# Optimization experiments

Measured on AMD Instinct MI355X. Metric: run time of the kernel, lower is better.

Reference implementation:

```python
import jax, jax.numpy as jnp
import numpy as np
from jax.ops import segment_sum, segment_max

N_NODES = 50000
N_GRAPHS = 64
EPS = 1e-16


def gat_layer(x, src, dst, W, a_src, a_dst, b, n_nodes):
    # PyG GATConv, heads=1: shared linear, additive attention, per-dst softmax
    h = x @ W                                  # [N, H]
    al_s = h @ a_src                           # [N]
    al_d = h @ a_dst                           # [N]
    e = jax.nn.leaky_relu(al_s[src] + al_d[dst], 0.2)   # [E]
    # numerically stable segment softmax over edges grouped by dst
    m = segment_max(e, dst, num_segments=n_nodes)
    m = jnp.where(jnp.isfinite(m), m, 0.0)
    ex = jnp.exp(e - m[dst])
    denom = segment_sum(ex, dst, num_segments=n_nodes)
    alpha = ex / (denom[dst] + EPS)            # [E]
    out = segment_sum(alpha[:, None] * h[src], dst, num_segments=n_nodes)
    return out + b


def setup_inputs() -> dict:
    key = jax.random.key(0)
    ks = jax.random.split(key, 16)
    H = 128
    x = jax.random.normal(ks[0], (N_NODES, 4), dtype=jnp.float32)
    edge_index = jax.random.randint(ks[1], (2, 800000), 0, N_NODES, dtype=jnp.int64)
    batch = jnp.sort(jax.random.randint(ks[2], (N_NODES,), 0, N_GRAPHS, dtype=jnp.int64))

    def glorot(k, shape):
        lim = np.sqrt(6.0 / (shape[0] + shape[-1]))
        return jax.random.uniform(k, shape, jnp.float32, -lim, lim)

    params = {
        'W1': glorot(ks[3], (4, H)), 'as1': glorot(ks[4], (H,)), 'ad1': glorot(ks[5], (H,)), 'b1': jnp.zeros((H,), jnp.float32),
        'W2': glorot(ks[6], (H, H)), 'as2': glorot(ks[7], (H,)), 'ad2': glorot(ks[8], (H,)), 'b2': jnp.zeros((H,), jnp.float32),
        'W3': glorot(ks[9], (H, H)), 'as3': glorot(ks[10], (H,)), 'ad3': glorot(ks[11], (H,)), 'b3': jnp.zeros((H,), jnp.float32),
        'Wlin': glorot(ks[12], (H, 2)), 'blin': jnp.zeros((2,), jnp.float32),
    }
    return {'x': x, 'edge_index': edge_index, 'batch': batch, **params}


def reference(x, edge_index, batch, W1, as1, ad1, b1, W2, as2, ad2, b2, W3, as3, ad3, b3, Wlin, blin):
    n = x.shape[0]
    # GATConv default add_self_loops=True
    loop = jnp.arange(n, dtype=edge_index.dtype)
    src = jnp.concatenate([edge_index[0], loop])
    dst = jnp.concatenate([edge_index[1], loop])

    h = jax.nn.relu(gat_layer(x, src, dst, W1, as1, ad1, b1, n))
    h = jax.nn.relu(gat_layer(h, src, dst, W2, as2, ad2, b2, n))
    h = gat_layer(h, src, dst, W3, as3, ad3, b3, n)

    # global_mean_pool
    sums = segment_sum(h, batch, num_segments=N_GRAPHS)          # [G, H]
    cnt = segment_sum(jnp.ones((n,), h.dtype), batch, num_segments=N_GRAPHS)
    pooled = sums / jnp.maximum(cnt, 1.0)[:, None]
    # dropout p=0.5 is identity in eval mode
    return pooled @ Wlin + blin                                   # [G, 2]
```

## Files before the change

kernel.cpp:

```cpp
#include <hip/hip_runtime.h>
#include <math.h>


#define BW 512
#define PART_CHUNK 4096

typedef __attribute__((ext_vector_type(8))) short short8v;
typedef __attribute__((ext_vector_type(4))) float f32x4;

__device__ __forceinline__ float bflo(unsigned u) { return __uint_as_float(u << 16); }
__device__ __forceinline__ float bfhi(unsigned u) { return __uint_as_float(u & 0xffff0000u); }
__device__ __forceinline__ unsigned pk2bf(float a, float b) {
  unsigned ua = __float_as_uint(a); ua += 0x7fffu + ((ua >> 16) & 1u);
  unsigned ub = __float_as_uint(b); ub += 0x7fffu + ((ub >> 16) & 1u);
  return (ua >> 16) | (ub & 0xffff0000u);
}

__global__ __launch_bounds__(256) void kb_hist(const int* __restrict__ ei,
                                               int* __restrict__ bcnt,
                                               int E, int ET, int NB) {
  __shared__ int h[128];
  int tid = threadIdx.x;
  if (tid < 128) h[tid] = 0;
  __syncthreads();
  int stride = gridDim.x * 256;
  for (int i = blockIdx.x * 256 + tid; i < ET; i += stride) {
    int dst = (i < E) ? ei[E + i] : (i - E);
    atomicAdd(&h[dst >> 9], 1);
  }
  __syncthreads();
  if (tid < NB && h[tid] > 0) atomicAdd(&bcnt[tid], h[tid]);
}

__global__ __launch_bounds__(128) void kb_scan(const int* __restrict__ bcnt,
                                               int* __restrict__ bbase,
                                               int* __restrict__ bcur,
                                               int* __restrict__ rowp,
                                               int N, int ET, int NB) {
  __shared__ int sm[128];
  int t = threadIdx.x;
  int v = (t < NB) ? bcnt[t] : 0;
  sm[t] = v;
  __syncthreads();
  for (int off = 1; off < 128; off <<= 1) {
    int u = (t >= off) ? sm[t - off] : 0;
    __syncthreads();
    sm[t] += u;
    __syncthreads();
  }
  int pre = sm[t] - v;
  if (t <= NB) bbase[t] = pre;
  if (t < NB) bcur[t] = pre;
  if (t == 0) rowp[N] = ET;
}

__global__ __launch_bounds__(256) void kb_part(const int* __restrict__ ei,
                                               int* __restrict__ bcur,
                                               int* __restrict__ bucketed,
                                               int E, int ET, int NB) {
  __shared__ int hist[128];
  __shared__ int runb[128];
  int tid = threadIdx.x;
  int base = blockIdx.x * PART_CHUNK;
  if (tid < 128) hist[tid] = 0;

  int sv[16], dv[16];
#pragma unroll
  for (int k = 0; k < 16; ++k) {
    int j = base + k * 256 + tid;
    int s = -1, d = 0;
    if (j < ET) {
      if (j < E) { s = ei[j]; d = ei[E + j]; }
      else       { s = j - E; d = j - E; }
    }
    sv[k] = s; dv[k] = d;
  }
  __syncthreads();
#pragma unroll
  for (int k = 0; k < 16; ++k)
    if (sv[k] >= 0) atomicAdd(&hist[dv[k] >> 9], 1);
  __syncthreads();
  if (tid < NB && hist[tid] > 0) runb[tid] = atomicAdd(&bcur[tid], hist[tid]);
  __syncthreads();
  if (tid < 128) hist[tid] = 0;
  __syncthreads();
#pragma unroll
  for (int k = 0; k < 16; ++k) {
    if (sv[k] >= 0) {
      int b = dv[k] >> 9;
      int off = atomicAdd(&hist[b], 1);
      bucketed[runb[b] + off] = (sv[k] << 9) | (dv[k] & (BW - 1));
    }
  }
}

__global__ __launch_bounds__(256) void kb_csr(const int* __restrict__ bucketed,
                                              const int* __restrict__ bbase,
                                              int* __restrict__ rowp,
                                              int* __restrict__ csr,
                                              int N) {
  __shared__ int h[512];
  __shared__ int sm[256];
  __shared__ int cur[512];
  int tid = threadIdx.x;
  int b = blockIdx.x;
  int cb = bbase[b], ce = bbase[b + 1];

  h[tid] = 0; h[tid + 256] = 0;
  __syncthreads();
  for (int j = cb + tid; j < ce; j += 256)
    atomicAdd(&h[bucketed[j] & (BW - 1)], 1);
  __syncthreads();
  int a0 = h[2 * tid], a1 = h[2 * tid + 1];
  int s = a0 + a1;
  sm[tid] = s;
  __syncthreads();
  for (int off = 1; off < 256; off <<= 1) {
    int u = (tid >= off) ? sm[tid - off] : 0;
    __syncthreads();
    sm[tid] += u;
    __syncthreads();
  }
  int pre = sm[tid] - s;
  cur[2 * tid] = pre;
  cur[2 * tid + 1] = pre + a0;
  __syncthreads();
  int node0 = b * BW;
  for (int local = tid; local < BW; local += 256) {
    int node = node0 + local;
    if (node < N) rowp[node] = cb + cur[local];
  }
  __syncthreads();
  for (int j = cb + tid; j < ce; j += 256) {
    int p = bucketed[j];
    int loc = p & (BW - 1);
    int pos = cb + atomicAdd(&cur[loc], 1);
    csr[pos] = (unsigned)p >> 9;
  }
}

__global__ __launch_bounds__(256) void k_prep(const float* __restrict__ W2,
                                              const float* __restrict__ W3,
                                              unsigned short* __restrict__ Wcm2,
                                              unsigned short* __restrict__ Wcm3) {
  int i = blockIdx.x * 256 + threadIdx.x;
  if (i < 16384) {
    int k = i >> 7, n = i & 127;
    unsigned u = __float_as_uint(W2[i]); u += 0x7fffu + ((u >> 16) & 1u);
    Wcm2[n * 128 + k] = (unsigned short)(u >> 16);
    unsigned v = __float_as_uint(W3[i]); v += 0x7fffu + ((v >> 16) & 1u);
    Wcm3[n * 128 + k] = (unsigned short)(v >> 16);
  }
}

__global__ __launch_bounds__(256) void k_gemm4al(const float* __restrict__ X,
                                                 const float* __restrict__ W,
                                                 const float* __restrict__ asv,
                                                 const float* __restrict__ adv,
                                                 unsigned* __restrict__ Hbf,
                                                 float* __restrict__ al_s,
                                                 float* __restrict__ al_d, int N) {
  int wid = threadIdx.x >> 6, lane = threadIdx.x & 63;
  int node = blockIdx.x * 4 + wid;
  if (node >= N) return;
  float4 xv = *(const float4*)(X + node * 4);
  int f = lane * 2;
  float2 w0 = *(const float2*)(W + f);
  float2 w1 = *(const float2*)(W + 128 + f);
  float2 w2 = *(const float2*)(W + 256 + f);
  float2 w3 = *(const float2*)(W + 384 + f);
  float h0 = xv.x * w0.x + xv.y * w1.x + xv.z * w2.x + xv.w * w3.x;
  float h1 = xv.x * w0.y + xv.y * w1.y + xv.z * w2.y + xv.w * w3.y;
  Hbf[node * 64 + lane] = pk2bf(h0, h1);
  float2 s2 = *(const float2*)(asv + f);
  float2 d2 = *(const float2*)(adv + f);
  float ps = h0 * s2.x + h1 * s2.y;
  float pd = h0 * d2.x + h1 * d2.y;
  for (int off = 32; off; off >>= 1) {
    ps += __shfl_xor(ps, off);
    pd += __shfl_xor(pd, off);
  }
  if (lane == 0) { al_s[node] = ps; al_d[node] = pd; }
}

__global__ __launch_bounds__(256) void k_gemm128mfma(
    const unsigned short* __restrict__ Xbf,
    const unsigned short* __restrict__ Wcm,
    const float* __restrict__ asv, const float* __restrict__ adv,
    unsigned* __restrict__ Hbf,
    float* __restrict__ al_s, float* __restrict__ al_d, int N) {
  int wid = threadIdx.x >> 6, lane = threadIdx.x & 63;
  int c = lane & 15, g = lane >> 4;
  int row0 = blockIdx.x * 64 + wid * 16;
  int arow = row0 + c;
  int arowc = (arow < N) ? arow : (N - 1);

  short8v a[4];
#pragma unroll
  for (int kt = 0; kt < 4; ++kt)
    a[kt] = *(const short8v*)(Xbf + (size_t)arowc * 128 + kt * 32 + g * 8);

  f32x4 acc[8];
#pragma unroll
  for (int f = 0; f < 8; ++f) acc[f] = (f32x4){0.f, 0.f, 0.f, 0.f};

#pragma unroll
  for (int f = 0; f < 8; ++f) {
    const unsigned short* wb = Wcm + (size_t)(f * 16 + c) * 128 + g * 8;
#pragma unroll
    for (int kt = 0; kt < 4; ++kt) {
      short8v b = *(const short8v*)(wb + kt * 32);
      acc[f] = __builtin_amdgcn_mfma_f32_16x16x32_bf16(a[kt], b, acc[f], 0, 0, 0);
    }
  }

  float ps[4] = {0.f, 0.f, 0.f, 0.f}, pd[4] = {0.f, 0.f, 0.f, 0.f};
#pragma unroll
  for (int f = 0; f < 8; ++f) {
    float as_c = asv[f * 16 + c], ad_c = adv[f * 16 + c];
#pragma unroll
    for (int j = 0; j < 4; ++j) { ps[j] += acc[f][j] * as_c; pd[j] += acc[f][j] * ad_c; }
  }
#pragma unroll
  for (int j = 0; j < 4; ++j) {
    for (int off = 1; off < 16; off <<= 1) {
      ps[j] += __shfl_xor(ps[j], off);
      pd[j] += __shfl_xor(pd[j], off);
    }
  }
  if (c == 0) {
#pragma unroll
    for (int j = 0; j < 4; ++j) {
      int r = row0 + g * 4 + j;
      if (r < N) { al_s[r] = ps[j]; al_d[r] = pd[j]; }
    }
  }

#pragma unroll
  for (int f = 0; f < 8; ++f) {
#pragma unroll
    for (int j = 0; j < 4; ++j) {
      float partner = __shfl_xor(acc[f][j], 1);
      int r = row0 + g * 4 + j;
      if (((lane & 1) == 0) && r < N)
        Hbf[(size_t)r * 64 + f * 8 + (c >> 1)] = pk2bf(acc[f][j], partner);
    }
  }
}

__global__ __launch_bounds__(256) void k_agg(const int* __restrict__ csr_src,
                                             const int* __restrict__ rowp,
                                             const float* __restrict__ al_s,
                                             const float* __restrict__ al_d,
                                             const uint4* __restrict__ Hbf,
                                             const float* __restrict__ bias,
                                             float* __restrict__ exw,
                                             float* __restrict__ Yf32,
                                             uint4* __restrict__ Ybf,
                                             int N, int relu) {
  int wid = threadIdx.x >> 6, lane = threadIdx.x & 63;
  int dst = blockIdx.x * 4 + wid;
  if (dst >= N) return;
  int beg = rowp[dst], end = rowp[dst + 1];
  int deg = end - beg;
  float ald = al_d[dst];

  int q = lane >> 4;
  int l = lane & 15;
  float acc[8];
#pragma unroll
  for (int c = 0; c < 8; ++c) acc[c] = 0.f;

  if (deg <= 64) {
    int srcv = 0;
    float e = -INFINITY;
    if (lane < deg) {
      srcv = csr_src[beg + lane];
      e = al_s[srcv] + ald;
      e = (e > 0.f) ? e : 0.2f * e;
    }
    float m = e;
    for (int off = 32; off; off >>= 1) m = fmaxf(m, __shfl_xor(m, off));
    float av = (lane < deg) ? __expf(e - m) : 0.f;
    float den = av;
    for (int off = 32; off; off >>= 1) den += __shfl_xor(den, off);
    av *= 1.0f / (den + 1e-16f);

    int t = 0;
    for (; t + 8 <= deg; t += 8) {
      int sA = __shfl(srcv, t + q);
      int sB = __shfl(srcv, t + 4 + q);
      float wA = __shfl(av, t + q);
      float wB = __shfl(av, t + 4 + q);
      uint4 va = Hbf[(size_t)sA * 16 + l];
      uint4 vb = Hbf[(size_t)sB * 16 + l];
      acc[0] += wA * bflo(va.x) + wB * bflo(vb.x);
      acc[1] += wA * bfhi(va.x) + wB * bfhi(vb.x);
      acc[2] += wA * bflo(va.y) + wB * bflo(vb.y);
      acc[3] += wA * bfhi(va.y) + wB * bfhi(vb.y);
      acc[4] += wA * bflo(va.z) + wB * bflo(vb.z);
      acc[5] += wA * bfhi(va.z) + wB * bfhi(vb.z);
      acc[6] += wA * bflo(va.w) + wB * bflo(vb.w);
      acc[7] += wA * bfhi(va.w) + wB * bfhi(vb.w);
    }
    if (t + 4 <= deg) {
      int sA = __shfl(srcv, t + q);
      float wA = __shfl(av, t + q);
      uint4 va = Hbf[(size_t)sA * 16 + l];
      acc[0] += wA * bflo(va.x); acc[1] += wA * bfhi(va.x);
      acc[2] += wA * bflo(va.y); acc[3] += wA * bfhi(va.y);
      acc[4] += wA * bflo(va.z); acc[5] += wA * bfhi(va.z);
      acc[6] += wA * bflo(va.w); acc[7] += wA * bfhi(va.w);
      t += 4;
    }
    {
      int sA = __shfl(srcv, t + q);
      float wA = __shfl(av, t + q);
      if (t + q < deg) {
        uint4 va = Hbf[(size_t)sA * 16 + l];
        acc[0] += wA * bflo(va.x); acc[1] += wA * bfhi(va.x);
        acc[2] += wA * bflo(va.y); acc[3] += wA * bfhi(va.y);
        acc[4] += wA * bflo(va.z); acc[5] += wA * bfhi(va.z);
        acc[6] += wA * bflo(va.w); acc[7] += wA * bfhi(va.w);
      }
    }
  } else {
    float m = -INFINITY;
    for (int j = beg + lane; j < end; j += 64) {
      float e = al_s[csr_src[j]] + ald;
      e = (e > 0.f) ? e : 0.2f * e;
      exw[j] = e;
      m = fmaxf(m, e);
    }
    for (int off = 32; off; off >>= 1) m = fmaxf(m, __shfl_xor(m, off));

    float den = 0.f;
    for (int j = beg + lane; j < end; j += 64) {
      float ex = __expf(exw[j] - m);
      exw[j] = ex;
      den += ex;
    }
    for (int off = 32; off; off >>= 1) den += __shfl_xor(den, off);
    float inv = 1.0f / (den + 1e-16f);

    for (int j = beg + q; j < end; j += 4) {
      int sA = csr_src[j];
      float wA = exw[j] * inv;
      uint4 va = Hbf[(size_t)sA * 16 + l];
      acc[0] += wA * bflo(va.x); acc[1] += wA * bfhi(va.x);
      acc[2] += wA * bflo(va.y); acc[3] += wA * bfhi(va.y);
      acc[4] += wA * bflo(va.z); acc[5] += wA * bfhi(va.z);
      acc[6] += wA * bflo(va.w); acc[7] += wA * bfhi(va.w);
    }
  }

#pragma unroll
  for (int c = 0; c < 8; ++c) {
    acc[c] += __shfl_xor(acc[c], 16);
    acc[c] += __shfl_xor(acc[c], 32);
  }
  if (q == 0) {
    float4 bv0 = *(const float4*)(bias + l * 8);
    float4 bv1 = *(const float4*)(bias + l * 8 + 4);
    float o0 = acc[0] + bv0.x, o1 = acc[1] + bv0.y, o2 = acc[2] + bv0.z, o3 = acc[3] + bv0.w;
    float o4 = acc[4] + bv1.x, o5 = acc[5] + bv1.y, o6 = acc[6] + bv1.z, o7 = acc[7] + bv1.w;
    if (relu) {
      o0 = fmaxf(o0, 0.f); o1 = fmaxf(o1, 0.f); o2 = fmaxf(o2, 0.f); o3 = fmaxf(o3, 0.f);
      o4 = fmaxf(o4, 0.f); o5 = fmaxf(o5, 0.f); o6 = fmaxf(o6, 0.f); o7 = fmaxf(o7, 0.f);
      uint4 pb;
      pb.x = pk2bf(o0, o1); pb.y = pk2bf(o2, o3);
      pb.z = pk2bf(o4, o5); pb.w = pk2bf(o6, o7);
      Ybf[(size_t)dst * 16 + l] = pb;
    } else {
      float4 w0 = make_float4(o0, o1, o2, o3);
      float4 w1 = make_float4(o4, o5, o6, o7);
      *(float4*)(Yf32 + (size_t)dst * 128 + l * 8) = w0;
      *(float4*)(Yf32 + (size_t)dst * 128 + l * 8 + 4) = w1;
    }
  }
}

__global__ __launch_bounds__(256) void k_pool(const float* __restrict__ Hh,
                                              const int* __restrict__ batch,
                                              float* __restrict__ gsum,
                                              float* __restrict__ gcnt,
                                              int N, int nwaves) {
  int gw = (blockIdx.x * 256 + threadIdx.x) >> 6;
  int lane = threadIdx.x & 63;
  int chunk = (N + nwaves - 1) / nwaves;
  int beg = gw * chunk;
  int end = beg + chunk; if (end > N) end = N;
  if (beg >= end) return;

  int curg = batch[beg];
  float2 acc = {0.f, 0.f};
  int cnt = 0;
  for (int n = beg; n < end; ++n) {
    int g = batch[n];
    if (g != curg) {
      atomicAdd(&gsum[curg * 128 + lane * 2], acc.x);
      atomicAdd(&gsum[curg * 128 + lane * 2 + 1], acc.y);
      if (lane == 0) atomicAdd(&gcnt[curg], (float)cnt);
      acc.x = 0.f; acc.y = 0.f; cnt = 0; curg = g;
    }
    float2 h = *(const float2*)(Hh + (size_t)n * 128 + lane * 2);
    acc.x += h.x; acc.y += h.y; ++cnt;
  }
  atomicAdd(&gsum[curg * 128 + lane * 2], acc.x);
  atomicAdd(&gsum[curg * 128 + lane * 2 + 1], acc.y);
  if (lane == 0) atomicAdd(&gcnt[curg], (float)cnt);
}

__global__ __launch_bounds__(128) void k_final(const float* __restrict__ gsum,
                                               const float* __restrict__ gcnt,
                                               const float* __restrict__ Wlin,
                                               const float* __restrict__ blin,
                                               float* __restrict__ out) {
  int t = threadIdx.x;
  int g = t >> 1, c = t & 1;
  float inv = 1.0f / fmaxf(gcnt[g], 1.0f);
  float acc = blin[c];
  for (int k = 0; k < 128; ++k) acc += gsum[g * 128 + k] * inv * Wlin[k * 2 + c];
  out[g * 2 + c] = acc;
}

extern "C" void kernel_launch(void* const* d_in, const int* in_sizes, int n_in,
                              void* d_out, int out_size, void* d_ws, size_t ws_size,
                              hipStream_t stream) {
  const float* x    = (const float*)d_in[0];
  const int*   ei   = (const int*)d_in[1];
  const int*   batch= (const int*)d_in[2];
  const float* W1   = (const float*)d_in[3];
  const float* as1  = (const float*)d_in[4];
  const float* ad1  = (const float*)d_in[5];
  const float* b1   = (const float*)d_in[6];
  const float* W2   = (const float*)d_in[7];
  const float* as2  = (const float*)d_in[8];
  const float* ad2  = (const float*)d_in[9];
  const float* b2   = (const float*)d_in[10];
  const float* W3   = (const float*)d_in[11];
  const float* as3  = (const float*)d_in[12];
  const float* ad3  = (const float*)d_in[13];
  const float* b3   = (const float*)d_in[14];
  const float* Wlin = (const float*)d_in[15];
  const float* blin = (const float*)d_in[16];

  int N = in_sizes[0] / 4;
  int E = in_sizes[1] / 2;
  int ET = E + N;
  int NB = (N + BW - 1) / BW;

  char* ws = (char*)d_ws;
  unsigned* bfA = (unsigned*)ws; ws += (size_t)N * 64 * 4;
  unsigned* bfB = (unsigned*)ws; ws += (size_t)N * 64 * 4;
  float* bufY = (float*)ws; ws += (size_t)N * 128 * 4;
  float* al_s = (float*)ws; ws += (size_t)N * 4;
  float* al_d = (float*)ws; ws += (size_t)N * 4;
  float* gsum = (float*)ws; ws += (size_t)64 * 128 * 4;
  float* gcnt = (float*)ws; ws += (size_t)64 * 4;
  int* rowp   = (int*)ws;   ws += (size_t)(N + 1) * 4;
  int* csr    = (int*)ws;   ws += (size_t)ET * 4;
  float* exw  = (float*)ws; ws += (size_t)ET * 4;
  int* bucketed = (int*)ws; ws += (size_t)ET * 4;
  int* bcnt   = (int*)ws;   ws += (size_t)128 * 4;
  int* bbase  = (int*)ws;   ws += (size_t)132 * 4;
  int* bcur   = (int*)ws;   ws += (size_t)128 * 4;
  unsigned short* wcm2 = (unsigned short*)ws; ws += (size_t)128 * 128 * 2;
  unsigned short* wcm3 = (unsigned short*)ws; ws += (size_t)128 * 128 * 2;

  hipMemsetAsync(bcnt, 0, (size_t)128 * 4, stream);
  hipMemsetAsync(gsum, 0, (size_t)(64 * 128 + 64) * 4, stream);

  kb_hist<<<256, 256, 0, stream>>>(ei, bcnt, E, ET, NB);
  kb_scan<<<1, 128, 0, stream>>>(bcnt, bbase, bcur, rowp, N, ET, NB);
  kb_part<<<(ET + PART_CHUNK - 1) / PART_CHUNK, 256, 0, stream>>>(ei, bcur, bucketed, E, ET, NB);
  kb_csr <<<NB, 256, 0, stream>>>(bucketed, bbase, rowp, csr, N);
  k_prep <<<64, 256, 0, stream>>>(W2, W3, wcm2, wcm3);

  int nb4 = (N + 3) / 4;
  int nb64 = (N + 63) / 64;
  k_gemm4al<<<nb4, 256, 0, stream>>>(x, W1, as1, ad1, bfA, al_s, al_d, N);
  k_agg    <<<nb4, 256, 0, stream>>>(csr, rowp, al_s, al_d, (const uint4*)bfA, b1, exw, bufY, (uint4*)bfB, N, 1);
  k_gemm128mfma<<<nb64, 256, 0, stream>>>((const unsigned short*)bfB, wcm2, as2, ad2, bfA, al_s, al_d, N);
  k_agg        <<<nb4, 256, 0, stream>>>(csr, rowp, al_s, al_d, (const uint4*)bfA, b2, exw, bufY, (uint4*)bfB, N, 1);
  k_gemm128mfma<<<nb64, 256, 0, stream>>>((const unsigned short*)bfB, wcm3, as3, ad3, bfA, al_s, al_d, N);
  k_agg        <<<nb4, 256, 0, stream>>>(csr, rowp, al_s, al_d, (const uint4*)bfA, b3, exw, bufY, (uint4*)bfB, N, 0);

  k_pool <<<256, 256, 0, stream>>>(bufY, batch, gsum, gcnt, N, 1024);
  k_final<<<1, 128, 0, stream>>>(gsum, gcnt, Wlin, blin, (float*)d_out);
}
```

Before: 346.9 us.

## Reorder layer-1 GAT to aggregate 4-dim inputs before the linear projection

```diff
diff --git a/kernel.cpp b/kernel.cpp
--- a/kernel.cpp
+++ b/kernel.cpp
@@ -153,34 +153,127 @@
   }
 }
 
-__global__ __launch_bounds__(256) void k_gemm4al(const float* __restrict__ X,
-                                                 const float* __restrict__ W,
-                                                 const float* __restrict__ asv,
-                                                 const float* __restrict__ adv,
-                                                 unsigned* __restrict__ Hbf,
-                                                 float* __restrict__ al_s,
-                                                 float* __restrict__ al_d, int N) {
+__global__ __launch_bounds__(64) void k_al1(const float* __restrict__ W1,
+                                            const float* __restrict__ as1,
+                                            const float* __restrict__ ad1,
+                                            float* __restrict__ wv) {
+  int lane = threadIdx.x;
+  float2 a = *(const float2*)(as1 + lane * 2);
+  float2 d = *(const float2*)(ad1 + lane * 2);
+  float ps[4], pd[4];
+#pragma unroll
+  for (int k = 0; k < 4; ++k) {
+    float2 w = *(const float2*)(W1 + k * 128 + lane * 2);
+    ps[k] = w.x * a.x + w.y * a.y;
+    pd[k] = w.x * d.x + w.y * d.y;
+  }
+  for (int off = 32; off; off >>= 1) {
+#pragma unroll
+    for (int k = 0; k < 4; ++k) {
+      ps[k] += __shfl_xor(ps[k], off);
+      pd[k] += __shfl_xor(pd[k], off);
+    }
+  }
+  if (lane == 0) {
+#pragma unroll
+    for (int k = 0; k < 4; ++k) { wv[k] = ps[k]; wv[4 + k] = pd[k]; }
+  }
+}
+
+__global__ __launch_bounds__(256) void k_alnode(const float* __restrict__ X,
+                                                const float* __restrict__ wv,
+                                                float* __restrict__ al_s,
+                                                float* __restrict__ al_d, int N) {
+  int i = blockIdx.x * 256 + threadIdx.x;
+  if (i >= N) return;
+  float4 xv = *(const float4*)(X + i * 4);
+  al_s[i] = xv.x * wv[0] + xv.y * wv[1] + xv.z * wv[2] + xv.w * wv[3];
+  al_d[i] = xv.x * wv[4] + xv.y * wv[5] + xv.z * wv[6] + xv.w * wv[7];
+}
+
+__global__ __launch_bounds__(256) void k_aggx(const int* __restrict__ csr_src,
+                                              const int* __restrict__ rowp,
+                                              const float* __restrict__ al_s,
+                                              const float* __restrict__ al_d,
+                                              const float* __restrict__ X,
+                                              float* __restrict__ exw,
+                                              float* __restrict__ AX, int N) {
+  int wid = threadIdx.x >> 6, lane = threadIdx.x & 63;
+  int dst = blockIdx.x * 4 + wid;
+  if (dst >= N) return;
+  int beg = rowp[dst], end = rowp[dst + 1];
+  int deg = end - beg;
+  float ald = al_d[dst];
+  float4 acc = {0.f, 0.f, 0.f, 0.f};
+
+  if (deg <= 64) {
+    int srcv = 0;
+    float e = -INFINITY;
+    if (lane < deg) {
+      srcv = csr_src[beg + lane];
+      e = al_s[srcv] + ald;
+      e = (e > 0.f) ? e : 0.2f * e;
+    }
+    float m = e;
+    for (int off = 32; off; off >>= 1) m = fmaxf(m, __shfl_xor(m, off));
+    float av = (lane < deg) ? __expf(e - m) : 0.f;
+    float den = av;
+    for (int off = 32; off; off >>= 1) den += __shfl_xor(den, off);
+    av *= 1.0f / (den + 1e-16f);
+    float4 xv = {0.f, 0.f, 0.f, 0.f};
+    if (lane < deg) xv = *(const float4*)(X + (size_t)srcv * 4);
+    acc.x = av * xv.x; acc.y = av * xv.y; acc.z = av * xv.z; acc.w = av * xv.w;
+  } else {
+    float m = -INFINITY;
+    for (int j = beg + lane; j < end; j += 64) {
+      float e = al_s[csr_src[j]] + ald;
+      e = (e > 0.f) ? e : 0.2f * e;
+      exw[j] = e;
+      m = fmaxf(m, e);
+    }
+    for (int off = 32; off; off >>= 1) m = fmaxf(m, __shfl_xor(m, off));
+    float den = 0.f;
+    for (int j = beg + lane; j < end; j += 64) {
+      float ex = __expf(exw[j] - m);
+      exw[j] = ex;
+      den += ex;
+    }
+    for (int off = 32; off; off >>= 1) den += __shfl_xor(den, off);
+    float inv = 1.0f / (den + 1e-16f);
+    for (int j = beg + lane; j < end; j += 64) {
+      int s = csr_src[j];
+      float w = exw[j] * inv;
+      float4 xv = *(const float4*)(X + (size_t)s * 4);
+      acc.x += w * xv.x; acc.y += w * xv.y; acc.z += w * xv.z; acc.w += w * xv.w;
+    }
+  }
+  for (int off = 32; off; off >>= 1) {
+    acc.x += __shfl_xor(acc.x, off);
+    acc.y += __shfl_xor(acc.y, off);
+    acc.z += __shfl_xor(acc.z, off);
+    acc.w += __shfl_xor(acc.w, off);
+  }
+  if (lane == 0) *(float4*)(AX + (size_t)dst * 4) = acc;
+}
+
+__global__ __launch_bounds__(256) void k_gemm4b(const float* __restrict__ AX,
+                                                const float* __restrict__ W,
+                                                const float* __restrict__ bias,
+                                                unsigned* __restrict__ Ybf, int N) {
   int wid = threadIdx.x >> 6, lane = threadIdx.x & 63;
   int node = blockIdx.x * 4 + wid;
   if (node >= N) return;
-  float4 xv = *(const float4*)(X + node * 4);
+  float4 xv = *(const float4*)(AX + (size_t)node * 4);
   int f = lane * 2;
   float2 w0 = *(const float2*)(W + f);
   float2 w1 = *(const float2*)(W + 128 + f);
   float2 w2 = *(const float2*)(W + 256 + f);
   float2 w3 = *(const float2*)(W + 384 + f);
-  float h0 = xv.x * w0.x + xv.y * w1.x + xv.z * w2.x + xv.w * w3.x;
-  float h1 = xv.x * w0.y + xv.y * w1.y + xv.z * w2.y + xv.w * w3.y;
-  Hbf[node * 64 + lane] = pk2bf(h0, h1);
-  float2 s2 = *(const float2*)(asv + f);
-  float2 d2 = *(const float2*)(adv + f);
-  float ps = h0 * s2.x + h1 * s2.y;
-  float pd = h0 * d2.x + h1 * d2.y;
-  for (int off = 32; off; off >>= 1) {
-    ps += __shfl_xor(ps, off);
-    pd += __shfl_xor(pd, off);
-  }
-  if (lane == 0) { al_s[node] = ps; al_d[node] = pd; }
+  float2 bv = *(const float2*)(bias + f);
+  float h0 = xv.x * w0.x + xv.y * w1.x + xv.z * w2.x + xv.w * w3.x + bv.x;
+  float h1 = xv.x * w0.y + xv.y * w1.y + xv.z * w2.y + xv.w * w3.y + bv.y;
+  h0 = fmaxf(h0, 0.f); h1 = fmaxf(h1, 0.f);
+  Ybf[(size_t)node * 64 + lane] = pk2bf(h0, h1);
 }
 
 __global__ __launch_bounds__(256) void k_gemm128mfma(
@@ -287,7 +380,29 @@
     av *= 1.0f / (den + 1e-16f);
 
     int t = 0;
-    for (; t + 8 <= deg; t += 8) {
+    for (; t + 16 <= deg; t += 16) {
+      int s0 = __shfl(srcv, t + q);
+      int s1 = __shfl(srcv, t + 4 + q);
+      int s2 = __shfl(srcv, t + 8 + q);
+      int s3 = __shfl(srcv, t + 12 + q);
+      float w0 = __shfl(av, t + q);
+      float w1 = __shfl(av, t + 4 + q);
+      float w2 = __shfl(av, t + 8 + q);
+      float w3 = __shfl(av, t + 12 + q);
+      uint4 v0 = Hbf[(size_t)s0 * 16 + l];
+      uint4 v1 = Hbf[(size_t)s1 * 16 + l];
+      uint4 v2 = Hbf[(size_t)s2 * 16 + l];
+      uint4 v3 = Hbf[(size_t)s3 * 16 + l];
+      acc[0] += w0 * bflo(v0.x) + w1 * bflo(v1.x) + w2 * bflo(v2.x) + w3 * bflo(v3.x);
+      acc[1] += w0 * bfhi(v0.x) + w1 * bfhi(v1.x) + w2 * bfhi(v2.x) + w3 * bfhi(v3.x);
+      acc[2] += w0 * bflo(v0.y) + w1 * bflo(v1.y) + w2 * bflo(v2.y) + w3 * bflo(v3.y);
+      acc[3] += w0 * bfhi(v0.y) + w1 * bfhi(v1.y) + w2 * bfhi(v2.y) + w3 * bfhi(v3.y);
+      acc[4] += w0 * bflo(v0.z) + w1 * bflo(v1.z) + w2 * bflo(v2.z) + w3 * bflo(v3.z);
+      acc[5] += w0 * bfhi(v0.z) + w1 * bfhi(v1.z) + w2 * bfhi(v2.z) + w3 * bfhi(v3.z);
+      acc[6] += w0 * bflo(v0.w) + w1 * bflo(v1.w) + w2 * bflo(v2.w) + w3 * bflo(v3.w);
+      acc[7] += w0 * bfhi(v0.w) + w1 * bfhi(v1.w) + w2 * bfhi(v2.w) + w3 * bfhi(v3.w);
+    }
+    if (t + 8 <= deg) {
       int sA = __shfl(srcv, t + q);
       int sB = __shfl(srcv, t + 4 + q);
       float wA = __shfl(av, t + q);
@@ -302,6 +417,7 @@
       acc[5] += wA * bfhi(va.z) + wB * bfhi(vb.z);
       acc[6] += wA * bflo(va.w) + wB * bflo(vb.w);
       acc[7] += wA * bfhi(va.w) + wB * bfhi(vb.w);
+      t += 8;
     }
     if (t + 4 <= deg) {
       int sA = __shfl(srcv, t + q);
@@ -456,8 +572,10 @@
   float* bufY = (float*)ws; ws += (size_t)N * 128 * 4;
   float* al_s = (float*)ws; ws += (size_t)N * 4;
   float* al_d = (float*)ws; ws += (size_t)N * 4;
+  float* AX   = (float*)ws; ws += (size_t)N * 4 * 4;
   float* gsum = (float*)ws; ws += (size_t)64 * 128 * 4;
   float* gcnt = (float*)ws; ws += (size_t)64 * 4;
+  float* wv   = (float*)ws; ws += (size_t)64 * 4;
   int* rowp   = (int*)ws;   ws += (size_t)(N + 1) * 4;
   int* csr    = (int*)ws;   ws += (size_t)ET * 4;
   float* exw  = (float*)ws; ws += (size_t)ET * 4;
@@ -476,11 +594,13 @@
   kb_part<<<(ET + PART_CHUNK - 1) / PART_CHUNK, 256, 0, stream>>>(ei, bcur, bucketed, E, ET, NB);
   kb_csr <<<NB, 256, 0, stream>>>(bucketed, bbase, rowp, csr, N);
   k_prep <<<64, 256, 0, stream>>>(W2, W3, wcm2, wcm3);
+  k_al1  <<<1, 64, 0, stream>>>(W1, as1, ad1, wv);
 
   int nb4 = (N + 3) / 4;
   int nb64 = (N + 63) / 64;
-  k_gemm4al<<<nb4, 256, 0, stream>>>(x, W1, as1, ad1, bfA, al_s, al_d, N);
-  k_agg    <<<nb4, 256, 0, stream>>>(csr, rowp, al_s, al_d, (const uint4*)bfA, b1, exw, bufY, (uint4*)bfB, N, 1);
+  k_alnode<<<(N + 255) / 256, 256, 0, stream>>>(x, wv, al_s, al_d, N);
+  k_aggx  <<<nb4, 256, 0, stream>>>(csr, rowp, al_s, al_d, x, exw, AX, N);
+  k_gemm4b<<<nb4, 256, 0, stream>>>(AX, W1, b1, bfB, N);
   k_gemm128mfma<<<nb64, 256, 0, stream>>>((const unsigned short*)bfB, wcm2, as2, ad2, bfA, al_s, al_d, N);
   k_agg        <<<nb4, 256, 0, stream>>>(csr, rowp, al_s, al_d, (const uint4*)bfA, b2, exw, bufY, (uint4*)bfB, N, 1);
   k_gemm128mfma<<<nb64, 256, 0, stream>>>((const unsigned short*)bfB, wcm3, as3, ad3, bfA, al_s, al_d, N);
```

Result: faster. 330.7 us (-4.7%).
